# Kernel tuning notes

Hardware: AMD Instinct MI355X
Metric: run time of the kernel (lower is better)

Reference implementation:

```python
import jax, jax.numpy as jnp
import numpy as np

DIM = 512
NUM_HEADS = 16
HEAD_DIM = DIM // NUM_HEADS
WINDOW = 256
MEM = 16  # memory tokens
NEG_INF = -1e30


def setup_inputs() -> dict:
    key = jax.random.key(0)
    ks = jax.random.split(key, 12)
    B, S, D = 2, 2048, DIM
    inp = {
        "query": jax.random.normal(ks[0], (B, S, D), jnp.float32),
        "key": jax.random.normal(ks[1], (B, S, D), jnp.float32),
        "value": jax.random.normal(ks[2], (B, S, D), jnp.float32),
        # persistent memory tokens, init N(0, 0.02)
        "mem": 0.02 * jax.random.normal(ks[3], (1, MEM, D), jnp.float32),
        # linear layers (stored as [in, out]; x @ W + b)
        "Wq": jax.random.normal(ks[4], (D, D), jnp.float32) / np.sqrt(D),
        "bq": jnp.zeros((D,), jnp.float32),
        "Wk": jax.random.normal(ks[5], (D, D), jnp.float32) / np.sqrt(D),
        "bk": jnp.zeros((D,), jnp.float32),
        "Wv": jax.random.normal(ks[6], (D, D), jnp.float32) / np.sqrt(D),
        "bv": jnp.zeros((D,), jnp.float32),
        "Wo": jax.random.normal(ks[7], (D, D), jnp.float32) / np.sqrt(D),
        "bo": jnp.zeros((D,), jnp.float32),
    }
    return inp


def _sliding_mask(seq_len):
    # additive mask for [MEM + seq_len] tokens: memory rows/cols fully visible,
    # content-content limited to |i-j| <= window//2
    T = seq_len + MEM
    w2 = WINDOW // 2
    i = jnp.arange(T)[:, None]
    j = jnp.arange(T)[None, :]
    allowed = (i < MEM) | (j < MEM) | (jnp.abs(i - j) <= w2)
    return jnp.where(allowed, 0.0, NEG_INF).astype(jnp.float32)


def reference(query, key, value, mem, Wq, bq, Wk, bk, Wv, bv, Wo, bo):
    B, S, D = query.shape
    scale = HEAD_DIM ** -0.5
    m = jnp.broadcast_to(mem, (B, MEM, D))
    qm = jnp.concatenate([m, query], axis=1)  # [B, T, D]
    km = jnp.concatenate([m, key], axis=1)
    vm = jnp.concatenate([m, value], axis=1)
    T = S + MEM

    def heads(x, W, b):
        y = x @ W + b
        return y.reshape(B, T, NUM_HEADS, HEAD_DIM).transpose(0, 2, 1, 3)  # [B,H,T,hd]

    q = heads(qm, Wq, bq)
    k = heads(km, Wk, bk)
    v = heads(vm, Wv, bv)

    mask = _sliding_mask(S)[None, None]  # [1,1,T,T]
    scores = jnp.einsum("bhqd,bhkd->bhqk", q, k) * scale + mask
    weights = jax.nn.softmax(scores, axis=-1)
    ctx = jnp.einsum("bhqk,bhkd->bhqd", weights, v)
    ctx = ctx.transpose(0, 2, 1, 3).reshape(B, T, D)
    ctx = ctx[:, MEM:]  # drop memory tokens
    return ctx @ Wo + bo
```

## Files before the change

kernel.cpp:

```cpp
#include <hip/hip_runtime.h>
#include <hip/hip_bf16.h>
#include <hip/hip_fp16.h>

#define DIM 512
#define NUM_HEADS 16
#define HEAD_DIM 32
#define WHALF 128
#define MEMN 16
#define SEQ 2048
#define BATCH 2
#define T_TOT (SEQ + MEMN)
#define MROWS (BATCH * T_TOT)
#define OROWS (BATCH * SEQ)
#define QT 128
#define MAXU 416
#define KSTR 40
#define VPLANE (MAXU * 16 * 2)

typedef _Float16 f16x8 __attribute__((ext_vector_type(8)));
typedef __fp16   f16raw2 __attribute__((ext_vector_type(2)));
typedef float    f32x4 __attribute__((ext_vector_type(4)));
typedef uint     u32x2 __attribute__((ext_vector_type(2)));

#define QSCALE 0.17677669529663687f

__device__ __forceinline__ u32x2 tr64(uint addr) {
    u32x2 r;
    asm volatile("ds_read_b64_tr_b16 %0, %1" : "=v"(r) : "v"(addr));
    return r;
}

__global__ __launch_bounds__(256) void prep_cvt(
    const float* __restrict__ q, const float* __restrict__ k,
    const float* __restrict__ v, const float* __restrict__ memp,
    const float* __restrict__ Wq, const float* __restrict__ Wk,
    const float* __restrict__ Wv, const float* __restrict__ Wo,
    ushort* __restrict__ Xq, ushort* __restrict__ Xk, ushort* __restrict__ Xv,
    ushort* __restrict__ Wtq, ushort* __restrict__ Wtk,
    ushort* __restrict__ Wtv, ushort* __restrict__ Wto)
{
    const int z = blockIdx.z;
    if (z < 3) {
        const float* X = z == 0 ? q : (z == 1 ? k : v);
        ushort*     Xc = z == 0 ? Xq : (z == 1 ? Xk : Xv);
        const int gid  = blockIdx.x * 256 + threadIdx.x;
        const int base = gid * 8;
        if (base >= MROWS * DIM) return;
        const int row = base >> 9;
        const int c   = base & 511;
        const int b   = row / T_TOT;
        const int t   = row - b * T_TOT;
        const float* src = (t < MEMN)
            ? (memp + (size_t)t * DIM + c)
            : (X + ((size_t)b * SEQ + (t - MEMN)) * DIM + c);
        const float4 a0 = *(const float4*)src;
        const float4 a1 = *(const float4*)(src + 4);
        union { _Float16 hh[8]; uint4 u4; } o;
        o.hh[0] = (_Float16)a0.x; o.hh[1] = (_Float16)a0.y;
        o.hh[2] = (_Float16)a0.z; o.hh[3] = (_Float16)a0.w;
        o.hh[4] = (_Float16)a1.x; o.hh[5] = (_Float16)a1.y;
        o.hh[6] = (_Float16)a1.z; o.hh[7] = (_Float16)a1.w;
        *(uint4*)(Xc + (size_t)row * DIM + c) = o.u4;
        return;
    }
    if (blockIdx.x >= 64) return;
    const int w = z - 3;
    const float* W  = w == 0 ? Wq  : (w == 1 ? Wk  : (w == 2 ? Wv  : Wo));
    ushort*     Wt  = w == 0 ? Wtq : (w == 1 ? Wtk : (w == 2 ? Wtv : Wto));
    const float ws  = (w == 0) ? QSCALE : 1.0f;

    __shared__ float sT[64][65];
    const int n0 = (blockIdx.x & 7) * 64;
    const int k0 = (blockIdx.x >> 3) * 64;

    for (int e = threadIdx.x; e < 1024; e += 256) {
        const int r  = e >> 4;
        const int c4 = e & 15;
        const float4 f = *(const float4*)(W + (size_t)(k0 + r) * DIM + n0 + c4 * 4);
        sT[r][c4 * 4 + 0] = f.x;
        sT[r][c4 * 4 + 1] = f.y;
        sT[r][c4 * 4 + 2] = f.z;
        sT[r][c4 * 4 + 3] = f.w;
    }
    __syncthreads();
    for (int u = threadIdx.x; u < 512; u += 256) {
        const int n  = u >> 3;
        const int kg = u & 7;
        union { ushort us[8]; uint4 u4; } o;
        #pragma unroll
        for (int j = 0; j < 8; ++j) {
            _Float16 h = (_Float16)(sT[kg * 8 + j][n] * ws);
            o.us[j] = *(ushort*)&h;
        }
        *(uint4*)(Wt + (size_t)(n0 + n) * DIM + k0 + kg * 8) = o.u4;
    }
}

template<bool OUT_HALF>
__device__ __forceinline__ void gemm_body64(
    const ushort* __restrict__ A, const ushort* __restrict__ Bt,
    const float* __restrict__ bias, float bscale, void* __restrict__ C, int M)
{
    __shared__ _Float16 sA[64][72];
    __shared__ _Float16 sB[128][72];

    const int tid  = threadIdx.x;
    const int row0 = blockIdx.x * 64;
    const int col0 = blockIdx.y * 128;
    const int wave = tid >> 6, lane = tid & 63;
    const int wr = wave >> 1, wc = wave & 1;
    const int fr = lane & 15, fq = lane >> 4;

    f32x4 acc[2][4];
    #pragma unroll
    for (int n = 0; n < 4; ++n) {
        const float bb = bias[col0 + wc * 64 + n * 16 + fr] * bscale;
        #pragma unroll
        for (int m = 0; m < 2; ++m) acc[m][n] = (f32x4){bb, bb, bb, bb};
    }

    for (int k0 = 0; k0 < 512; k0 += 64) {
        __syncthreads();
        #pragma unroll
        for (int it = 0; it < 6; ++it) {
            const int u  = tid + it * 256;
            const int cc = u & 7;
            if (u < 512) {
                const int r = u >> 3;
                int gr = row0 + r; if (gr >= M) gr = M - 1;
                *(uint4*)&sA[r][cc * 8] =
                    *(const uint4*)(A + (size_t)gr * 512 + k0 + cc * 8);
            } else {
                const int r = (u - 512) >> 3;
                *(uint4*)&sB[r][cc * 8] =
                    *(const uint4*)(Bt + (size_t)(col0 + r) * 512 + k0 + cc * 8);
            }
        }
        __syncthreads();
        #pragma unroll
        for (int kk = 0; kk < 2; ++kk) {
            f16x8 a[2], b[4];
            #pragma unroll
            for (int m = 0; m < 2; ++m)
                a[m] = *(const f16x8*)&sA[wr * 32 + m * 16 + fr][kk * 32 + fq * 8];
            #pragma unroll
            for (int n = 0; n < 4; ++n)
                b[n] = *(const f16x8*)&sB[wc * 64 + n * 16 + fr][kk * 32 + fq * 8];
            #pragma unroll
            for (int m = 0; m < 2; ++m)
                #pragma unroll
                for (int n = 0; n < 4; ++n)
                    acc[m][n] = __builtin_amdgcn_mfma_f32_16x16x32_f16(
                        a[m], b[n], acc[m][n], 0, 0, 0);
        }
    }

    #pragma unroll
    for (int m = 0; m < 2; ++m)
        #pragma unroll
        for (int n = 0; n < 4; ++n)
            #pragma unroll
            for (int j = 0; j < 4; ++j) {
                const int row = row0 + wr * 32 + m * 16 + fq * 4 + j;
                const int col = col0 + wc * 64 + n * 16 + fr;
                if (row < M) {
                    if (OUT_HALF) {
                        _Float16 h = (_Float16)acc[m][n][j];
                        ((ushort*)C)[(size_t)row * 512 + col] = *(ushort*)&h;
                    } else {
                        ((float*)C)[(size_t)row * 512 + col] = acc[m][n][j];
                    }
                }
            }
}

__global__ __launch_bounds__(256) void gemm_qkv(
    const ushort* __restrict__ Xq, const ushort* __restrict__ Xk,
    const ushort* __restrict__ Xv,
    const ushort* __restrict__ Wtq, const ushort* __restrict__ Wtk,
    const ushort* __restrict__ Wtv,
    const float* __restrict__ bq, const float* __restrict__ bk,
    const float* __restrict__ bv,
    ushort* __restrict__ Qc, ushort* __restrict__ Kc, ushort* __restrict__ Vc)
{
    const int w = blockIdx.z;
    const ushort* A  = w == 0 ? Xq  : (w == 1 ? Xk  : Xv);
    const ushort* Bt = w == 0 ? Wtq : (w == 1 ? Wtk : Wtv);
    const float*  bi = w == 0 ? bq  : (w == 1 ? bk  : bv);
    ushort*       Cc = w == 0 ? Qc  : (w == 1 ? Kc  : Vc);
    gemm_body64<true>(A, Bt, bi, (w == 0) ? QSCALE : 1.0f, Cc, MROWS);
}

__global__ __launch_bounds__(256) void gemm_out64(
    const ushort* __restrict__ A, const ushort* __restrict__ Bt,
    const float* __restrict__ bias, float* __restrict__ C)
{
    gemm_body64<false>(A, Bt, bias, 1.0f, C, OROWS);
}

__global__ __launch_bounds__(512, 4) void attn_mfma(
    const ushort* __restrict__ Q, const ushort* __restrict__ K,
    const ushort* __restrict__ V, ushort* __restrict__ ctx)
{
    const int tid  = threadIdx.x;
    const int tile = blockIdx.x, h = blockIdx.y, b = blockIdx.z;
    const int wave = tid >> 6, lane = tid & 63;
    const int fr = lane & 15, fq = lane >> 4;
    const int fq8 = fq * 8, fq4 = fq * 4;

    const int i0  = MEMN + tile * QT;
    const int klo = max(MEMN, i0 - WHALF);
    const int khi = min(T_TOT - 1, i0 + QT - 1 + WHALF);
    const int total  = MEMN + khi - klo + 1;
    const int ustage = (total + 31) & ~31;

    __shared__ ushort sK[MAXU][KSTR];
    __shared__ ushort sV[2][MAXU][16];

    const size_t hbase = (size_t)b * T_TOT * DIM + (size_t)h * HEAD_DIM;

    for (int idx = tid; idx < ustage * 4; idx += 512) {
        const int u = idx >> 2, c = idx & 3;
        uint4 val = {0, 0, 0, 0};
        if (u < total) {
            const int g = (u < MEMN) ? u : klo + u - MEMN;
            val = *(const uint4*)(K + hbase + (size_t)g * DIM + c * 8);
        }
        *(uint4*)&sK[u][c * 8] = val;
    }
    for (int idx = tid; idx < ustage * 4; idx += 512) {
        const int pl   = (idx >= ustage * 2) ? 1 : 0;
        const int s    = idx - pl * ustage * 2;
        const int u    = s >> 1, half = s & 1;
        uint4 val = {0, 0, 0, 0};
        if (u < total) {
            const int g = (u < MEMN) ? u : klo + u - MEMN;
            val = *(const uint4*)(V + hbase + (size_t)g * DIM + pl * 16 + half * 8);
        }
        *(uint4*)&sV[pl][u][half * 8] = val;
    }

    const int iq = i0 + wave * 16 + fr;
    const f16x8 qf = *(const f16x8*)(Q + (size_t)(b * T_TOT + iq) * DIM
                                     + h * HEAD_DIM + fq8);

    const int ulo  = max(iq - WHALF - klo, 0) + MEMN;
    const int uhi  = min(iq + WHALF, khi) - klo + MEMN;
    const int span = uhi - ulo;
    const int iw0  = i0 + wave * 16;
    const int ulo_minw = max(iw0 - WHALF - klo, 0) + MEMN;
    const int ulo_maxw = max(iw0 + 15 - WHALF - klo, 0) + MEMN;
    const int uhi_minw = min(iw0 + WHALF, khi) - klo + MEMN;
    const int uhi_maxw = min(iw0 + 15 + WHALF, khi) - klo + MEMN;
    const int glo = max(1, ulo_minw >> 5);
    const int ghi = uhi_maxw >> 5;

    const uint vlane = (uint)(size_t)(&sV[0][0][0]) + (uint)(lane * 8);

    __syncthreads();

    const float NEGINF = -__builtin_huge_valf();
    float mns = 0.0f;
    float l   = 0.f;
    f32x4 oc0 = {0, 0, 0, 0}, oc1 = {0, 0, 0, 0};

    {
        const f16x8 kfA = *(const f16x8*)&sK[fr][fq8];
        const f16x8 kfB = *(const f16x8*)&sK[16 + fr][fq8];
        f32x4 sA = {0, 0, 0, 0}, sB = {0, 0, 0, 0};
        sA = __builtin_amdgcn_mfma_f32_16x16x32_f16(kfA, qf, sA, 0, 0, 0);
        sB = __builtin_amdgcn_mfma_f32_16x16x32_f16(kfB, qf, sB, 0, 0, 0);
        const uint vb = vlane;
        u32x2 t0 = tr64(vb), t1 = tr64(vb + 512);
        u32x2 t2 = tr64(vb + VPLANE), t3 = tr64(vb + VPLANE + 512);
        if (!(16 >= ulo_maxw && 31 <= uhi_minw)) {
            #pragma unroll
            for (int j = 0; j < 4; ++j) {
                const uint uu = (uint)(16 + fq4 + j - ulo);
                sB[j] = (uu <= (uint)span) ? sB[j] : NEGINF;
            }
        }
        float mx = fmaxf(fmaxf(fmaxf(sA[0], sA[1]), fmaxf(sA[2], sA[3])),
                         fmaxf(fmaxf(sB[0], sB[1]), fmaxf(sB[2], sB[3])));
        mx = fmaxf(mx, __shfl_xor(mx, 16));
        mx = fmaxf(mx, __shfl_xor(mx, 32));
        if (!__all(mx <= mns)) {
            const float mn2   = fmaxf(mns, mx);
            const float alpha = __expf(mns - mn2);
            l *= alpha;
            #pragma unroll
            for (int j = 0; j < 4; ++j) { oc0[j] *= alpha; oc1[j] *= alpha; }
            mns = mn2;
        }
        const float p0 = __expf(sA[0] - mns), p1 = __expf(sA[1] - mns);
        const float p2 = __expf(sA[2] - mns), p3 = __expf(sA[3] - mns);
        const float p4 = __expf(sB[0] - mns), p5 = __expf(sB[1] - mns);
        const float p6 = __expf(sB[2] - mns), p7 = __expf(sB[3] - mns);
        l += ((p0 + p1) + (p2 + p3)) + ((p4 + p5) + (p6 + p7));
        union { f16raw2 h2; uint u; } c0, c1, c2, c3;
        c0.h2 = __builtin_amdgcn_cvt_pkrtz(p0, p1);
        c1.h2 = __builtin_amdgcn_cvt_pkrtz(p2, p3);
        c2.h2 = __builtin_amdgcn_cvt_pkrtz(p4, p5);
        c3.h2 = __builtin_amdgcn_cvt_pkrtz(p6, p7);
        union { uint u[4]; f16x8 h; } P;
        P.u[0] = c0.u; P.u[1] = c1.u; P.u[2] = c2.u; P.u[3] = c3.u;
        asm volatile("s_waitcnt lgkmcnt(0)" ::: "memory");
        __builtin_amdgcn_sched_barrier(0);
        union { u32x2 d[2]; f16x8 h; } VA0, VA1;
        VA0.d[0] = t0; VA0.d[1] = t1;
        VA1.d[0] = t2; VA1.d[1] = t3;
        oc0 = __builtin_amdgcn_mfma_f32_16x16x32_f16(VA0.h, P.h, oc0, 0, 0, 0);
        oc1 = __builtin_amdgcn_mfma_f32_16x16x32_f16(VA1.h, P.h, oc1, 0, 0, 0);
    }

    int g = glo;
    for (; g + 1 <= ghi; g += 2) {
        const int ua = g * 32, ub2 = ua + 32;
        const f16x8 kf0 = *(const f16x8*)&sK[ua + fr][fq8];
        const f16x8 kf1 = *(const f16x8*)&sK[ua + 16 + fr][fq8];
        const f16x8 kf2 = *(const f16x8*)&sK[ub2 + fr][fq8];
        const f16x8 kf3 = *(const f16x8*)&sK[ub2 + 16 + fr][fq8];
        f32x4 s0 = {0,0,0,0}, s1 = {0,0,0,0}, s2 = {0,0,0,0}, s3 = {0,0,0,0};
        s0 = __builtin_amdgcn_mfma_f32_16x16x32_f16(kf0, qf, s0, 0, 0, 0);
        s1 = __builtin_amdgcn_mfma_f32_16x16x32_f16(kf1, qf, s1, 0, 0, 0);
        s2 = __builtin_amdgcn_mfma_f32_16x16x32_f16(kf2, qf, s2, 0, 0, 0);
        s3 = __builtin_amdgcn_mfma_f32_16x16x32_f16(kf3, qf, s3, 0, 0, 0);
        const uint vb = vlane + (uint)(ua * 32);
        u32x2 ta0 = tr64(vb),          ta1 = tr64(vb + 512);
        u32x2 ta2 = tr64(vb + VPLANE), ta3 = tr64(vb + VPLANE + 512);
        u32x2 tb0 = tr64(vb + 1024),          tb1 = tr64(vb + 1536);
        u32x2 tb2 = tr64(vb + VPLANE + 1024), tb3 = tr64(vb + VPLANE + 1536);
        #pragma unroll
        for (int cch = 0; cch < 4; ++cch) {
            const int base = ua + cch * 16;
            f32x4& sc = cch == 0 ? s0 : (cch == 1 ? s1 : (cch == 2 ? s2 : s3));
            if (!(base >= ulo_maxw && base + 15 <= uhi_minw)) {
                #pragma unroll
                for (int j = 0; j < 4; ++j) {
                    const uint uu = (uint)(base + fq4 + j - ulo);
                    sc[j] = (uu <= (uint)span) ? sc[j] : NEGINF;
                }
            }
        }
        float mxA = fmaxf(fmaxf(fmaxf(s0[0], s0[1]), fmaxf(s0[2], s0[3])),
                          fmaxf(fmaxf(s1[0], s1[1]), fmaxf(s1[2], s1[3])));
        float mxB = fmaxf(fmaxf(fmaxf(s2[0], s2[1]), fmaxf(s2[2], s2[3])),
                          fmaxf(fmaxf(s3[0], s3[1]), fmaxf(s3[2], s3[3])));
        float mx = fmaxf(mxA, mxB);
        mx = fmaxf(mx, __shfl_xor(mx, 16));
        mx = fmaxf(mx, __shfl_xor(mx, 32));
        if (!__all(mx <= mns)) {
            const float mn2   = fmaxf(mns, mx);
            const float alpha = __expf(mns - mn2);
            l *= alpha;
            #pragma unroll
            for (int j = 0; j < 4; ++j) { oc0[j] *= alpha; oc1[j] *= alpha; }
            mns = mn2;
        }
        const float a0 = __expf(s0[0] - mns), a1 = __expf(s0[1] - mns);
        const float a2 = __expf(s0[2] - mns), a3 = __expf(s0[3] - mns);
        const float a4 = __expf(s1[0] - mns), a5 = __expf(s1[1] - mns);
        const float a6 = __expf(s1[2] - mns), a7 = __expf(s1[3] - mns);
        const float b0 = __expf(s2[0] - mns), b1 = __expf(s2[1] - mns);
        const float b2 = __expf(s2[2] - mns), b3 = __expf(s2[3] - mns);
        const float b4 = __expf(s3[0] - mns), b5 = __expf(s3[1] - mns);
        const float b6 = __expf(s3[2] - mns), b7 = __expf(s3[3] - mns);
        l += (((a0 + a1) + (a2 + a3)) + ((a4 + a5) + (a6 + a7)))
           + (((b0 + b1) + (b2 + b3)) + ((b4 + b5) + (b6 + b7)));
        union { f16raw2 h2; uint u; } d0, d1, d2, d3, e0, e1, e2, e3;
        d0.h2 = __builtin_amdgcn_cvt_pkrtz(a0, a1);
        d1.h2 = __builtin_amdgcn_cvt_pkrtz(a2, a3);
        d2.h2 = __builtin_amdgcn_cvt_pkrtz(a4, a5);
        d3.h2 = __builtin_amdgcn_cvt_pkrtz(a6, a7);
        e0.h2 = __builtin_amdgcn_cvt_pkrtz(b0, b1);
        e1.h2 = __builtin_amdgcn_cvt_pkrtz(b2, b3);
        e2.h2 = __builtin_amdgcn_cvt_pkrtz(b4, b5);
        e3.h2 = __builtin_amdgcn_cvt_pkrtz(b6, b7);
        union { uint u[4]; f16x8 h; } P0, P1;
        P0.u[0] = d0.u; P0.u[1] = d1.u; P0.u[2] = d2.u; P0.u[3] = d3.u;
        P1.u[0] = e0.u; P1.u[1] = e1.u; P1.u[2] = e2.u; P1.u[3] = e3.u;
        asm volatile("s_waitcnt lgkmcnt(0)" ::: "memory");
        __builtin_amdgcn_sched_barrier(0);
        union { u32x2 d[2]; f16x8 h; } A0, A1, B0, B1;
        A0.d[0] = ta0; A0.d[1] = ta1;
        A1.d[0] = ta2; A1.d[1] = ta3;
        B0.d[0] = tb0; B0.d[1] = tb1;
        B1.d[0] = tb2; B1.d[1] = tb3;
        oc0 = __builtin_amdgcn_mfma_f32_16x16x32_f16(A0.h, P0.h, oc0, 0, 0, 0);
        oc1 = __builtin_amdgcn_mfma_f32_16x16x32_f16(A1.h, P0.h, oc1, 0, 0, 0);
        oc0 = __builtin_amdgcn_mfma_f32_16x16x32_f16(B0.h, P1.h, oc0, 0, 0, 0);
        oc1 = __builtin_amdgcn_mfma_f32_16x16x32_f16(B1.h, P1.h, oc1, 0, 0, 0);
    }
    if (g <= ghi) {
        const int ua = g * 32;
        const f16x8 kf0 = *(const f16x8*)&sK[ua + fr][fq8];
        const f16x8 kf1 = *(const f16x8*)&sK[ua + 16 + fr][fq8];
        f32x4 s0 = {0,0,0,0}, s1 = {0,0,0,0};
        s0 = __builtin_amdgcn_mfma_f32_16x16x32_f16(kf0, qf, s0, 0, 0, 0);
        s1 = __builtin_amdgcn_mfma_f32_16x16x32_f16(kf1, qf, s1, 0, 0, 0);
        const uint vb = vlane + (uint)(ua * 32);
        u32x2 t0 = tr64(vb),          t1 = tr64(vb + 512);
        u32x2 t2 = tr64(vb + VPLANE), t3 = tr64(vb + VPLANE + 512);
        #pragma unroll
        for (int cch = 0; cch < 2; ++cch) {
            const int base = ua + cch * 16;
            f32x4& sc = cch == 0 ? s0 : s1;
            if (!(base >= ulo_maxw && base + 15 <= uhi_minw)) {
                #pragma unroll
                for (int j = 0; j < 4; ++j) {
                    const uint uu = (uint)(base + fq4 + j - ulo);
                    sc[j] = (uu <= (uint)span) ? sc[j] : NEGINF;
                }
            }
        }
        float mx = fmaxf(fmaxf(fmaxf(s0[0], s0[1]), fmaxf(s0[2], s0[3])),
                         fmaxf(fmaxf(s1[0], s1[1]), fmaxf(s1[2], s1[3])));
        mx = fmaxf(mx, __shfl_xor(mx, 16));
        mx = fmaxf(mx, __shfl_xor(mx, 32));
        if (!__all(mx <= mns)) {
            const float mn2   = fmaxf(mns, mx);
            const float alpha = __expf(mns - mn2);
            l *= alpha;
            #pragma unroll
            for (int j = 0; j < 4; ++j) { oc0[j] *= alpha; oc1[j] *= alpha; }
            mns = mn2;
        }
        const float p0 = __expf(s0[0] - mns), p1 = __expf(s0[1] - mns);
        const float p2 = __expf(s0[2] - mns), p3 = __expf(s0[3] - mns);
        const float p4 = __expf(s1[0] - mns), p5 = __expf(s1[1] - mns);
        const float p6 = __expf(s1[2] - mns), p7 = __expf(s1[3] - mns);
        l += ((p0 + p1) + (p2 + p3)) + ((p4 + p5) + (p6 + p7));
        union { f16raw2 h2; uint u; } c0, c1, c2, c3;
        c0.h2 = __builtin_amdgcn_cvt_pkrtz(p0, p1);
        c1.h2 = __builtin_amdgcn_cvt_pkrtz(p2, p3);
        c2.h2 = __builtin_amdgcn_cvt_pkrtz(p4, p5);
        c3.h2 = __builtin_amdgcn_cvt_pkrtz(p6, p7);
        union { uint u[4]; f16x8 h; } P;
        P.u[0] = c0.u; P.u[1] = c1.u; P.u[2] = c2.u; P.u[3] = c3.u;
        asm volatile("s_waitcnt lgkmcnt(0)" ::: "memory");
        __builtin_amdgcn_sched_barrier(0);
        union { u32x2 d[2]; f16x8 h; } VA0, VA1;
        VA0.d[0] = t0; VA0.d[1] = t1;
        VA1.d[0] = t2; VA1.d[1] = t3;
        oc0 = __builtin_amdgcn_mfma_f32_16x16x32_f16(VA0.h, P.h, oc0, 0, 0, 0);
        oc1 = __builtin_amdgcn_mfma_f32_16x16x32_f16(VA1.h, P.h, oc1, 0, 0, 0);
    }

    l += __shfl_xor(l, 16);
    l += __shfl_xor(l, 32);
    const float inv = 1.0f / l;
    union { f16raw2 h2; uint u; } w00, w01, w10, w11;
    w00.h2 = __builtin_amdgcn_cvt_pkrtz(oc0[0] * inv, oc0[1] * inv);
    w01.h2 = __builtin_amdgcn_cvt_pkrtz(oc0[2] * inv, oc0[3] * inv);
    w10.h2 = __builtin_amdgcn_cvt_pkrtz(oc1[0] * inv, oc1[1] * inv);
    w11.h2 = __builtin_amdgcn_cvt_pkrtz(oc1[2] * inv, oc1[3] * inv);
    ushort* cp = ctx + ((size_t)b * SEQ + (iq - MEMN)) * DIM
               + h * HEAD_DIM + fq4;
    *(uint2*)cp        = (uint2){w00.u, w01.u};
    *(uint2*)(cp + 16) = (uint2){w10.u, w11.u};
}

extern "C" void kernel_launch(void* const* d_in, const int* in_sizes, int n_in,
                              void* d_out, int out_size, void* d_ws, size_t ws_size,
                              hipStream_t stream) {
    const float* q    = (const float*)d_in[0];
    const float* k    = (const float*)d_in[1];
    const float* v    = (const float*)d_in[2];
    const float* memp = (const float*)d_in[3];
    const float* Wq   = (const float*)d_in[4];
    const float* bq   = (const float*)d_in[5];
    const float* Wk   = (const float*)d_in[6];
    const float* bk   = (const float*)d_in[7];
    const float* Wv   = (const float*)d_in[8];
    const float* bv   = (const float*)d_in[9];
    const float* Wo   = (const float*)d_in[10];
    const float* bo   = (const float*)d_in[11];
    float* out = (float*)d_out;

    const size_t NX = (size_t)MROWS * DIM;
    const size_t NW = (size_t)DIM * DIM;
    const size_t NC = (size_t)OROWS * DIM;

    ushort* p   = (ushort*)d_ws;
    ushort* Xq  = p;            p += NX;
    ushort* Xk  = p;            p += NX;
    ushort* Xv  = p;            p += NX;
    ushort* Qc  = p;            p += NX;
    ushort* Kc  = p;            p += NX;
    ushort* Vc  = p;            p += NX;
    ushort* Wtq = p;            p += NW;
    ushort* Wtk = p;            p += NW;
    ushort* Wtv = p;            p += NW;
    ushort* Wto = p;            p += NW;
    ushort* Cc  = p;            p += NC;

    dim3 gp((MROWS * DIM / 8 + 255) / 256, 1, 7);
    prep_cvt<<<gp, 256, 0, stream>>>(q, k, v, memp, Wq, Wk, Wv, Wo,
                                     Xq, Xk, Xv, Wtq, Wtk, Wtv, Wto);

    dim3 g1((MROWS + 63) / 64, 4, 3);
    gemm_qkv<<<g1, 256, 0, stream>>>(Xq, Xk, Xv, Wtq, Wtk, Wtv,
                                     bq, bk, bv, Qc, Kc, Vc);

    dim3 g2(SEQ / QT, NUM_HEADS, BATCH);
    attn_mfma<<<g2, 512, 0, stream>>>(Qc, Kc, Vc, Cc);

    dim3 g3(OROWS / 64, 4, 1);
    gemm_out64<<<g3, 256, 0, stream>>>(Cc, Wto, bo, out);
}
```

Before: 65.34 us.

## Fuse input fp32-to-fp16 conversion into QKV GEMM and pre-swizzle weight fragments

Drops the separate pass that converted the q/k/v/mem activations to fp16; the QKV GEMM now reads fp32 rows directly and converts them while staging into shared memory. Weights are pre-arranged into MFMA B-fragment order, so each wave loads its B operands straight from global memory without shared-memory staging. The GEMMs are retiled so each block covers all 512 output columns (32 rows for QKV, 16 rows for the output projection), which removes an intermediate buffer and its write/read traffic. In exchange, B fragments are re-read from global/L2 by every block, and the new tiles have less reuse per block.

```diff
diff --git a/kernel.cpp b/kernel.cpp
--- a/kernel.cpp
+++ b/kernel.cpp
@@ -30,44 +30,16 @@
     return r;
 }
 
-__global__ __launch_bounds__(256) void prep_cvt(
-    const float* __restrict__ q, const float* __restrict__ k,
-    const float* __restrict__ v, const float* __restrict__ memp,
+__global__ __launch_bounds__(256) void prep_wfrag(
     const float* __restrict__ Wq, const float* __restrict__ Wk,
     const float* __restrict__ Wv, const float* __restrict__ Wo,
-    ushort* __restrict__ Xq, ushort* __restrict__ Xk, ushort* __restrict__ Xv,
-    ushort* __restrict__ Wtq, ushort* __restrict__ Wtk,
-    ushort* __restrict__ Wtv, ushort* __restrict__ Wto)
+    ushort* __restrict__ Fq, ushort* __restrict__ Fk,
+    ushort* __restrict__ Fv, ushort* __restrict__ Fo)
 {
-    const int z = blockIdx.z;
-    if (z < 3) {
-        const float* X = z == 0 ? q : (z == 1 ? k : v);
-        ushort*     Xc = z == 0 ? Xq : (z == 1 ? Xk : Xv);
-        const int gid  = blockIdx.x * 256 + threadIdx.x;
-        const int base = gid * 8;
-        if (base >= MROWS * DIM) return;
-        const int row = base >> 9;
-        const int c   = base & 511;
-        const int b   = row / T_TOT;
-        const int t   = row - b * T_TOT;
-        const float* src = (t < MEMN)
-            ? (memp + (size_t)t * DIM + c)
-            : (X + ((size_t)b * SEQ + (t - MEMN)) * DIM + c);
-        const float4 a0 = *(const float4*)src;
-        const float4 a1 = *(const float4*)(src + 4);
-        union { _Float16 hh[8]; uint4 u4; } o;
-        o.hh[0] = (_Float16)a0.x; o.hh[1] = (_Float16)a0.y;
-        o.hh[2] = (_Float16)a0.z; o.hh[3] = (_Float16)a0.w;
-        o.hh[4] = (_Float16)a1.x; o.hh[5] = (_Float16)a1.y;
-        o.hh[6] = (_Float16)a1.z; o.hh[7] = (_Float16)a1.w;
-        *(uint4*)(Xc + (size_t)row * DIM + c) = o.u4;
-        return;
-    }
-    if (blockIdx.x >= 64) return;
-    const int w = z - 3;
-    const float* W  = w == 0 ? Wq  : (w == 1 ? Wk  : (w == 2 ? Wv  : Wo));
-    ushort*     Wt  = w == 0 ? Wtq : (w == 1 ? Wtk : (w == 2 ? Wtv : Wto));
-    const float ws  = (w == 0) ? QSCALE : 1.0f;
+    const int w = blockIdx.z;
+    const float* W = w == 0 ? Wq : (w == 1 ? Wk : (w == 2 ? Wv : Wo));
+    ushort*     F  = w == 0 ? Fq : (w == 1 ? Fk : (w == 2 ? Fv : Fo));
+    const float ws = (w == 0) ? QSCALE : 1.0f;
 
     __shared__ float sT[64][65];
     const int n0 = (blockIdx.x & 7) * 64;
@@ -83,119 +55,161 @@
         sT[r][c4 * 4 + 3] = f.w;
     }
     __syncthreads();
-    for (int u = threadIdx.x; u < 512; u += 256) {
-        const int n  = u >> 3;
-        const int kg = u & 7;
-        union { ushort us[8]; uint4 u4; } o;
-        #pragma unroll
-        for (int j = 0; j < 8; ++j) {
-            _Float16 h = (_Float16)(sT[kg * 8 + j][n] * ws);
-            o.us[j] = *(ushort*)&h;
-        }
-        *(uint4*)(Wt + (size_t)(n0 + n) * DIM + k0 + kg * 8) = o.u4;
+    for (int e = threadIdx.x; e < 512; e += 256) {
+        const int nn   = e >> 7;
+        const int kss  = (e >> 6) & 1;
+        const int lane = e & 63;
+        const int fr = lane & 15, fq = lane >> 4;
+        union { _Float16 hh[8]; uint4 u4; } o;
+        #pragma unroll
+        for (int j = 0; j < 8; ++j)
+            o.hh[j] = (_Float16)(sT[kss * 32 + fq * 8 + j][nn * 16 + fr] * ws);
+        const size_t idx =
+            ((size_t)((n0 / 16 + nn) * 16 + (k0 / 32 + kss)) * 64 + lane) * 8;
+        *(uint4*)(F + idx) = o.u4;
     }
 }
 
-template<bool OUT_HALF>
-__device__ __forceinline__ void gemm_body64(
-    const ushort* __restrict__ A, const ushort* __restrict__ Bt,
-    const float* __restrict__ bias, float bscale, void* __restrict__ C, int M)
-{
-    __shared__ _Float16 sA[64][72];
-    __shared__ _Float16 sB[128][72];
-
-    const int tid  = threadIdx.x;
-    const int row0 = blockIdx.x * 64;
-    const int col0 = blockIdx.y * 128;
-    const int wave = tid >> 6, lane = tid & 63;
-    const int wr = wave >> 1, wc = wave & 1;
-    const int fr = lane & 15, fq = lane >> 4;
-
-    f32x4 acc[2][4];
-    #pragma unroll
-    for (int n = 0; n < 4; ++n) {
-        const float bb = bias[col0 + wc * 64 + n * 16 + fr] * bscale;
-        #pragma unroll
-        for (int m = 0; m < 2; ++m) acc[m][n] = (f32x4){bb, bb, bb, bb};
-    }
-
-    for (int k0 = 0; k0 < 512; k0 += 64) {
-        __syncthreads();
-        #pragma unroll
-        for (int it = 0; it < 6; ++it) {
-            const int u  = tid + it * 256;
-            const int cc = u & 7;
-            if (u < 512) {
-                const int r = u >> 3;
-                int gr = row0 + r; if (gr >= M) gr = M - 1;
-                *(uint4*)&sA[r][cc * 8] =
-                    *(const uint4*)(A + (size_t)gr * 512 + k0 + cc * 8);
-            } else {
-                const int r = (u - 512) >> 3;
-                *(uint4*)&sB[r][cc * 8] =
-                    *(const uint4*)(Bt + (size_t)(col0 + r) * 512 + k0 + cc * 8);
-            }
-        }
-        __syncthreads();
-        #pragma unroll
-        for (int kk = 0; kk < 2; ++kk) {
-            f16x8 a[2], b[4];
-            #pragma unroll
-            for (int m = 0; m < 2; ++m)
-                a[m] = *(const f16x8*)&sA[wr * 32 + m * 16 + fr][kk * 32 + fq * 8];
-            #pragma unroll
-            for (int n = 0; n < 4; ++n)
-                b[n] = *(const f16x8*)&sB[wc * 64 + n * 16 + fr][kk * 32 + fq * 8];
-            #pragma unroll
-            for (int m = 0; m < 2; ++m)
-                #pragma unroll
-                for (int n = 0; n < 4; ++n)
-                    acc[m][n] = __builtin_amdgcn_mfma_f32_16x16x32_f16(
-                        a[m], b[n], acc[m][n], 0, 0, 0);
-        }
-    }
-
-    #pragma unroll
-    for (int m = 0; m < 2; ++m)
-        #pragma unroll
-        for (int n = 0; n < 4; ++n)
-            #pragma unroll
-            for (int j = 0; j < 4; ++j) {
-                const int row = row0 + wr * 32 + m * 16 + fq * 4 + j;
-                const int col = col0 + wc * 64 + n * 16 + fr;
-                if (row < M) {
-                    if (OUT_HALF) {
-                        _Float16 h = (_Float16)acc[m][n][j];
-                        ((ushort*)C)[(size_t)row * 512 + col] = *(ushort*)&h;
-                    } else {
-                        ((float*)C)[(size_t)row * 512 + col] = acc[m][n][j];
-                    }
-                }
-            }
-}
-
-__global__ __launch_bounds__(256) void gemm_qkv(
-    const ushort* __restrict__ Xq, const ushort* __restrict__ Xk,
-    const ushort* __restrict__ Xv,
-    const ushort* __restrict__ Wtq, const ushort* __restrict__ Wtk,
-    const ushort* __restrict__ Wtv,
+__global__ __launch_bounds__(256) void gemm_qkv_f(
+    const float* __restrict__ q, const float* __restrict__ k,
+    const float* __restrict__ v, const float* __restrict__ memp,
+    const ushort* __restrict__ Fq, const ushort* __restrict__ Fk,
+    const ushort* __restrict__ Fv,
     const float* __restrict__ bq, const float* __restrict__ bk,
     const float* __restrict__ bv,
     ushort* __restrict__ Qc, ushort* __restrict__ Kc, ushort* __restrict__ Vc)
 {
     const int w = blockIdx.z;
-    const ushort* A  = w == 0 ? Xq  : (w == 1 ? Xk  : Xv);
-    const ushort* Bt = w == 0 ? Wtq : (w == 1 ? Wtk : Wtv);
-    const float*  bi = w == 0 ? bq  : (w == 1 ? bk  : bv);
-    ushort*       Cc = w == 0 ? Qc  : (w == 1 ? Kc  : Vc);
-    gemm_body64<true>(A, Bt, bi, (w == 0) ? QSCALE : 1.0f, Cc, MROWS);
+    const float*  X  = w == 0 ? q  : (w == 1 ? k  : v);
+    const ushort* F  = w == 0 ? Fq : (w == 1 ? Fk : Fv);
+    const float*  bi = w == 0 ? bq : (w == 1 ? bk : bv);
+    ushort*       Co = w == 0 ? Qc : (w == 1 ? Kc : Vc);
+    const float bscale = (w == 0) ? QSCALE : 1.0f;
+
+    __shared__ _Float16 sA[32][72];
+
+    const int tid  = threadIdx.x;
+    const int row0 = blockIdx.x * 32;
+    const int wave = tid >> 6, lane = tid & 63;
+    const int fr = lane & 15, fq = lane >> 4;
+    const int ncol0 = wave * 128;
+
+    f32x4 acc[2][8];
+    #pragma unroll
+    for (int n = 0; n < 8; ++n) {
+        const float bb = bi[ncol0 + n * 16 + fr] * bscale;
+        acc[0][n] = (f32x4){bb, bb, bb, bb};
+        acc[1][n] = (f32x4){bb, bb, bb, bb};
+    }
+
+    const int r  = tid >> 3, cc = tid & 7;
+    const int gr = row0 + r;
+    const int bb_ = gr >= T_TOT ? 1 : 0;
+    const int t   = gr - bb_ * T_TOT;
+    const float* srcrow = (t < MEMN)
+        ? (memp + (size_t)t * DIM)
+        : (X + ((size_t)bb_ * SEQ + (t - MEMN)) * DIM);
+
+    for (int step = 0; step < 8; ++step) {
+        const int k0 = step * 64;
+        __syncthreads();
+        {
+            const float* src = srcrow + k0 + cc * 8;
+            const float4 a0 = ((const float4*)src)[0];
+            const float4 a1 = ((const float4*)src)[1];
+            union { _Float16 hh[8]; uint4 u4; } o;
+            o.hh[0] = (_Float16)a0.x; o.hh[1] = (_Float16)a0.y;
+            o.hh[2] = (_Float16)a0.z; o.hh[3] = (_Float16)a0.w;
+            o.hh[4] = (_Float16)a1.x; o.hh[5] = (_Float16)a1.y;
+            o.hh[6] = (_Float16)a1.z; o.hh[7] = (_Float16)a1.w;
+            *(uint4*)&sA[r][cc * 8] = o.u4;
+        }
+        __syncthreads();
+        #pragma unroll
+        for (int kk = 0; kk < 2; ++kk) {
+            const int ks = step * 2 + kk;
+            f16x8 a[2], b[8];
+            #pragma unroll
+            for (int m = 0; m < 2; ++m)
+                a[m] = *(const f16x8*)&sA[m * 16 + fr][kk * 32 + fq * 8];
+            #pragma unroll
+            for (int n = 0; n < 8; ++n)
+                b[n] = *(const f16x8*)(F +
+                    ((size_t)((wave * 8 + n) * 16 + ks) * 64 + lane) * 8);
+            #pragma unroll
+            for (int m = 0; m < 2; ++m)
+                #pragma unroll
+                for (int n = 0; n < 8; ++n)
+                    acc[m][n] = __builtin_amdgcn_mfma_f32_16x16x32_f16(
+                        a[m], b[n], acc[m][n], 0, 0, 0);
+        }
+    }
+
+    #pragma unroll
+    for (int m = 0; m < 2; ++m)
+        #pragma unroll
+        for (int n = 0; n < 8; ++n)
+            #pragma unroll
+            for (int j = 0; j < 4; ++j) {
+                const int row = row0 + m * 16 + fq * 4 + j;
+                const int col = ncol0 + n * 16 + fr;
+                _Float16 h = (_Float16)acc[m][n][j];
+                Co[(size_t)row * 512 + col] = *(ushort*)&h;
+            }
 }
 
-__global__ __launch_bounds__(256) void gemm_out64(
-    const ushort* __restrict__ A, const ushort* __restrict__ Bt,
+__global__ __launch_bounds__(256) void gemm_out_f(
+    const ushort* __restrict__ A, const ushort* __restrict__ F,
     const float* __restrict__ bias, float* __restrict__ C)
 {
-    gemm_body64<false>(A, Bt, bias, 1.0f, C, OROWS);
+    __shared__ _Float16 sA[16][72];
+
+    const int tid  = threadIdx.x;
+    const int row0 = blockIdx.x * 16;
+    const int wave = tid >> 6, lane = tid & 63;
+    const int fr = lane & 15, fq = lane >> 4;
+    const int ncol0 = wave * 128;
+
+    f32x4 acc[8];
+    #pragma unroll
+    for (int n = 0; n < 8; ++n) {
+        const float bb = bias[ncol0 + n * 16 + fr];
+        acc[n] = (f32x4){bb, bb, bb, bb};
+    }
+
+    for (int step = 0; step < 8; ++step) {
+        const int k0 = step * 64;
+        __syncthreads();
+        if (tid < 128) {
+            const int r = tid >> 3, cc = tid & 7;
+            *(uint4*)&sA[r][cc * 8] =
+                *(const uint4*)(A + (size_t)(row0 + r) * 512 + k0 + cc * 8);
+        }
+        __syncthreads();
+        #pragma unroll
+        for (int kk = 0; kk < 2; ++kk) {
+            const int ks = step * 2 + kk;
+            const f16x8 a = *(const f16x8*)&sA[fr][kk * 32 + fq * 8];
+            f16x8 b[8];
+            #pragma unroll
+            for (int n = 0; n < 8; ++n)
+                b[n] = *(const f16x8*)(F +
+                    ((size_t)((wave * 8 + n) * 16 + ks) * 64 + lane) * 8);
+            #pragma unroll
+            for (int n = 0; n < 8; ++n)
+                acc[n] = __builtin_amdgcn_mfma_f32_16x16x32_f16(
+                    a, b[n], acc[n], 0, 0, 0);
+        }
+    }
+
+    #pragma unroll
+    for (int n = 0; n < 8; ++n)
+        #pragma unroll
+        for (int j = 0; j < 4; ++j) {
+            const int row = row0 + fq * 4 + j;
+            const int col = ncol0 + n * 16 + fr;
+            C[(size_t)row * 512 + col] = acc[n][j];
+        }
 }
 
 __global__ __launch_bounds__(512, 4) void attn_mfma(
@@ -482,29 +496,25 @@
     const size_t NC = (size_t)OROWS * DIM;
 
     ushort* p   = (ushort*)d_ws;
-    ushort* Xq  = p;            p += NX;
-    ushort* Xk  = p;            p += NX;
-    ushort* Xv  = p;            p += NX;
     ushort* Qc  = p;            p += NX;
     ushort* Kc  = p;            p += NX;
     ushort* Vc  = p;            p += NX;
-    ushort* Wtq = p;            p += NW;
-    ushort* Wtk = p;            p += NW;
-    ushort* Wtv = p;            p += NW;
-    ushort* Wto = p;            p += NW;
+    ushort* Fq  = p;            p += NW;
+    ushort* Fk  = p;            p += NW;
+    ushort* Fv  = p;            p += NW;
+    ushort* Fo  = p;            p += NW;
     ushort* Cc  = p;            p += NC;
 
-    dim3 gp((MROWS * DIM / 8 + 255) / 256, 1, 7);
-    prep_cvt<<<gp, 256, 0, stream>>>(q, k, v, memp, Wq, Wk, Wv, Wo,
-                                     Xq, Xk, Xv, Wtq, Wtk, Wtv, Wto);
-
-    dim3 g1((MROWS + 63) / 64, 4, 3);
-    gemm_qkv<<<g1, 256, 0, stream>>>(Xq, Xk, Xv, Wtq, Wtk, Wtv,
-                                     bq, bk, bv, Qc, Kc, Vc);
+    dim3 gw(64, 1, 4);
+    prep_wfrag<<<gw, 256, 0, stream>>>(Wq, Wk, Wv, Wo, Fq, Fk, Fv, Fo);
+
+    dim3 g1(MROWS / 32, 1, 3);
+    gemm_qkv_f<<<g1, 256, 0, stream>>>(q, k, v, memp, Fq, Fk, Fv,
+                                       bq, bk, bv, Qc, Kc, Vc);
 
     dim3 g2(SEQ / QT, NUM_HEADS, BATCH);
     attn_mfma<<<g2, 512, 0, stream>>>(Qc, Kc, Vc, Cc);
 
-    dim3 g3(OROWS / 64, 4, 1);
-    gemm_out64<<<g3, 256, 0, stream>>>(Cc, Wto, bo, out);
+    dim3 g3(OROWS / 16, 1, 1);
+    gemm_out_f<<<g3, 256, 0, stream>>>(Cc, Fo, bo, out);
 }
```

After: 73.51 us. +12.5%, slower.
